# Kernel optimization log

Hardware: AMD Instinct MI355X
Metric: run time of the kernel (lower is better)

Reference implementation:

```python
import jax, jax.numpy as jnp
import numpy as np

EPS = 1e-5


def _prelu(x, a):
    return jnp.where(x >= 0, x, a * x)


def _chan_ln(x, gamma, beta, axis):
    # LayerNormalization4D: normalize over the channel axis, affine per channel
    mu = jnp.mean(x, axis=axis, keepdims=True)
    var = jnp.var(x, axis=axis, keepdims=True)
    return (x - mu) / jnp.sqrt(var + EPS) * gamma + beta


def setup_inputs() -> dict:
    key = jax.random.key(0)
    ks = jax.random.split(key, 12)
    B, C, T, F = 2, 64, 3000, 65
    H, D = 4, 4            # n_head, hid_chan
    E = C // H             # per-head value channels
    s = lambda k, shape: (jax.random.normal(k, shape, jnp.float32) * 0.05)
    return dict(
        x=jax.random.normal(ks[0], (B, C, T, F), jnp.float32),
        # per-head 1x1-conv Q/K/V projections (stacked over head axis)
        Wq=s(ks[1], (H, D, C)), bq=s(ks[2], (H, D)),
        aq=jnp.full((H,), 0.25, jnp.float32),
        gq=jnp.ones((H, D), jnp.float32), betaq=jnp.zeros((H, D), jnp.float32),
        Wk=s(ks[3], (H, D, C)), bk=s(ks[4], (H, D)),
        ak=jnp.full((H,), 0.25, jnp.float32),
        gk=jnp.ones((H, D), jnp.float32), betak=jnp.zeros((H, D), jnp.float32),
        Wv=s(ks[5], (H, E, C)), bv=s(ks[6], (H, E)),
        av=jnp.full((H,), 0.25, jnp.float32),
        gv=jnp.ones((H, E), jnp.float32), betav=jnp.zeros((H, E), jnp.float32),
        # final concat 1x1-conv projection
        Wp=s(ks[7], (C, C)), bp=s(ks[8], (C,)),
        ap=jnp.asarray(0.25, jnp.float32),
        gp=jnp.ones((C,), jnp.float32), betap=jnp.zeros((C,), jnp.float32),
    )


def _conv_act_norm_heads(x, W, b, a, g, beta):
    # x: [B,C,T,F]; W: [H,O,C] -> y: [B,H,O,T,F]
    y = jnp.einsum('hoc,bctf->bhotf', W, x) + b[None, :, :, None, None]
    y = _prelu(y, a[None, :, None, None, None])
    return _chan_ln(y, g[None, :, :, None, None], beta[None, :, :, None, None], axis=2)


def reference(x, Wq, bq, aq, gq, betaq, Wk, bk, ak, gk, betak,
              Wv, bv, av, gv, betav, Wp, bp, ap, gp, betap):
    B, C, T, F = x.shape
    H = Wq.shape[0]
    D = Wq.shape[1]
    E = Wv.shape[1]

    q = _conv_act_norm_heads(x, Wq, bq, aq, gq, betaq)   # [B,H,D,T,F]
    k = _conv_act_norm_heads(x, Wk, bk, ak, gk, betak)   # [B,H,D,T,F]
    v = _conv_act_norm_heads(x, Wv, bv, av, gv, betav)   # [B,H,E,T,F]

    # flatten (chan, freq) -> embedding per time step
    Qf = q.transpose(0, 1, 3, 2, 4).reshape(B, H, T, D * F)
    Kf = k.transpose(0, 1, 3, 2, 4).reshape(B, H, T, D * F)
    Vf = v.transpose(0, 1, 3, 2, 4).reshape(B, H, T, E * F)

    scale = 1.0 / jnp.sqrt(jnp.asarray(D * F, x.dtype))
    attn = jax.nn.softmax(jnp.einsum('bhtd,bhsd->bhts', Qf, Kf) * scale, axis=-1)
    o = jnp.einsum('bhts,bhse->bhte', attn, Vf)          # [B,H,T,E*F]

    # un-flatten and concat heads along channel dim
    o = o.reshape(B, H, T, E, F).transpose(0, 1, 3, 2, 4).reshape(B, H * E, T, F)

    # final 1x1 conv + PReLU + channel LN, then residual
    y = jnp.einsum('oc,bctf->botf', Wp, o) + bp[None, :, None, None]
    y = _prelu(y, ap)
    y = _chan_ln(y, gp[None, :, None, None], betap[None, :, None, None], axis=1)
    return y + x
```

## Files before the change

kernel.cpp:

```cpp
#include <hip/hip_runtime.h>
#include <stdint.h>

#define B_ 2
#define C_ 64
#define T_ 3000
#define F_ 65
#define H_ 4
#define D_ 4
#define E_ 16
#define TF_ (T_*F_)
#define NPT (B_*TF_)
#define EF 1040
#define TP 3072
#define TK 3008
#define DQK 260
#define SQK 328
#define VTROWS 1152
#define ABUF 8192
#define BBUF 4096

typedef unsigned short u16;
typedef unsigned int   u32;
typedef __attribute__((ext_vector_type(8))) short  s16x8;
typedef __attribute__((ext_vector_type(4))) float  f32x4;
typedef __attribute__((ext_vector_type(4))) u32    u32x4;

__device__ __forceinline__ float bf2f(u16 u){ return __uint_as_float(((u32)u)<<16); }
__device__ __forceinline__ float bf2f_lo(u32 u){ return __uint_as_float(u<<16); }
__device__ __forceinline__ float bf2f_hi(u32 u){ return __uint_as_float(u & 0xffff0000u); }
__device__ __forceinline__ u16 f2bf(float f){
  u32 u = __float_as_uint(f);
  u32 r = u + 0x7fffu + ((u>>16)&1u);
  return (u16)(r>>16);
}

__device__ __forceinline__ void gld16(const u16* g, u16* l){
  __builtin_amdgcn_global_load_lds((const __attribute__((address_space(1))) u32*)g,
                                   (__attribute__((address_space(3))) u32*)l,
                                   16, 0, 0);
}

__global__ __launch_bounds__(256) void qkv_kernel(
    const float* __restrict__ x,
    const float* __restrict__ Wq, const float* __restrict__ bq, const float* __restrict__ aq,
    const float* __restrict__ gq, const float* __restrict__ bteq,
    const float* __restrict__ Wk, const float* __restrict__ bk, const float* __restrict__ ak,
    const float* __restrict__ gk, const float* __restrict__ btek,
    const float* __restrict__ Wv, const float* __restrict__ bv, const float* __restrict__ av,
    const float* __restrict__ gv, const float* __restrict__ btev,
    u16* __restrict__ Qf, u16* __restrict__ Kf, u16* __restrict__ Vf,
    float* __restrict__ lbuf)
{
  __shared__ __align__(16) u16 wlds[2*96*64];
  const int tid = threadIdx.x;
  for (int i = tid; i < 6144; i += 256){
    const int row = i >> 6, c = i & 63;
    float w;
    if (row < 16)      w = Wq[row*64 + c];
    else if (row < 32) w = Wk[(row-16)*64 + c];
    else               w = Wv[(row-32)*64 + c];
    const u16 hi = f2bf(w);
    const u16 lo = f2bf(w - bf2f(hi));
    const int byo = ((row<<7) + (c<<1)) ^ ((row&7)<<4);
    *(u16*)((char*)wlds + byo)         = hi;
    *(u16*)((char*)wlds + 12288 + byo) = lo;
  }
  const int gid = blockIdx.x*256 + tid;
  if (gid < 8*TP) lbuf[gid] = 0.f;
  __syncthreads();

  const int wv_ = tid >> 6, l = tid & 63;
  const int lm = l & 15, lq = l >> 4;
  const int p0 = blockIdx.x*128 + wv_*32;

  int bb[2], rr[2]; bool ok[2];
  #pragma unroll
  for (int nt=0; nt<2; nt++){
    int p = p0 + nt*16 + lm;
    ok[nt] = (p < NPT);
    if (p >= NPT) p = NPT-1;
    bb[nt] = (p >= TF_) ? 1 : 0;
    rr[nt] = p - bb[nt]*TF_;
  }

  f32x4 acc[6][2];
  #pragma unroll
  for (int i=0;i<6;i++){
    acc[i][0]=(f32x4){0.f,0.f,0.f,0.f};
    acc[i][1]=(f32x4){0.f,0.f,0.f,0.f};
  }

  #pragma unroll
  for (int ks=0; ks<2; ks++){
    const int c0 = ks*32 + lq*8;
    s16x8 xhi[2], xlo[2];
    #pragma unroll
    for (int nt=0; nt<2; nt++){
      const float* xb = x + ((size_t)bb[nt]*C_ + c0)*TF_ + rr[nt];
      float xr[8];
      #pragma unroll
      for (int j=0;j<8;j++) xr[j] = xb[(size_t)j*TF_];
      u32x4 hw, lw;
      #pragma unroll
      for (int jw=0;jw<4;jw++){
        const u16 h0 = f2bf(xr[jw*2+0]);
        const u16 h1 = f2bf(xr[jw*2+1]);
        const float r0 = xr[jw*2+0] - bf2f(h0);
        const float r1 = xr[jw*2+1] - bf2f(h1);
        hw[jw] = (u32)h0 | ((u32)h1<<16);
        lw[jw] = (u32)f2bf(r0) | ((u32)f2bf(r1)<<16);
      }
      xhi[nt] = __builtin_bit_cast(s16x8, hw);
      xlo[nt] = __builtin_bit_cast(s16x8, lw);
    }
    #pragma unroll
    for (int mt=0; mt<6; mt++){
      const int rowb = mt*16 + lm;
      const int byo = ((rowb<<7) + (c0<<1)) ^ ((rowb&7)<<4);
      const s16x8 whi = *(const s16x8*)((const char*)wlds + byo);
      const s16x8 wlo = *(const s16x8*)((const char*)wlds + 12288 + byo);
      #pragma unroll
      for (int nt=0; nt<2; nt++){
        acc[mt][nt] = __builtin_amdgcn_mfma_f32_16x16x32_bf16(whi, xhi[nt], acc[mt][nt], 0,0,0);
        acc[mt][nt] = __builtin_amdgcn_mfma_f32_16x16x32_bf16(whi, xlo[nt], acc[mt][nt], 0,0,0);
        acc[mt][nt] = __builtin_amdgcn_mfma_f32_16x16x32_bf16(wlo, xhi[nt], acc[mt][nt], 0,0,0);
      }
    }
  }

  #pragma unroll
  for (int nt=0; nt<2; nt++){
    if (!ok[nt]) continue;
    const int b = bb[nt], r = rr[nt];
    const u32 t = (u32)(((unsigned long long)r * 516223ULL) >> 25);
    const int f = r - (int)t*65;
    {
      const int h = lq;
      const float a_ = aq[h];
      float v[4]; float s1 = 0.f;
      #pragma unroll
      for (int d=0; d<4; d++){
        float a = acc[0][nt][d] + bq[h*4+d];
        a = (a >= 0.f) ? a : a_*a;
        v[d] = a; s1 += a;
      }
      const float mu = s1*0.25f;
      float var = 0.f;
      #pragma unroll
      for (int d=0; d<4; d++){ const float dd = v[d]-mu; var = fmaf(dd,dd,var); }
      var *= 0.25f;
      const float rs = rsqrtf(var + 1e-5f);
      u16* qrow = Qf + ((size_t)(b*4+h)*TP + t)*SQK + f;
      #pragma unroll
      for (int d=0; d<4; d++)
        qrow[d*F_] = f2bf((v[d]-mu)*rs*gq[h*4+d] + bteq[h*4+d]);
    }
    {
      const int h = lq;
      const float a_ = ak[h];
      float v[4]; float s1 = 0.f;
      #pragma unroll
      for (int d=0; d<4; d++){
        float a = acc[1][nt][d] + bk[h*4+d];
        a = (a >= 0.f) ? a : a_*a;
        v[d] = a; s1 += a;
      }
      const float mu = s1*0.25f;
      float var = 0.f;
      #pragma unroll
      for (int d=0; d<4; d++){ const float dd = v[d]-mu; var = fmaf(dd,dd,var); }
      var *= 0.25f;
      const float rs = rsqrtf(var + 1e-5f);
      u16* krow = Kf + ((size_t)(b*4+h)*TP + t)*SQK + f;
      #pragma unroll
      for (int d=0; d<4; d++)
        krow[d*F_] = f2bf((v[d]-mu)*rs*gk[h*4+d] + btek[h*4+d]);
    }
    if (f < 28) {
      #pragma unroll
      for (int h2=0; h2<4; h2++){
        Qf[((size_t)(b*4+h2)*TP + t)*SQK + 260 + f] = 0;
        Kf[((size_t)(b*4+h2)*TP + t)*SQK + 260 + f] = 0;
      }
    }
    #pragma unroll
    for (int mt=2; mt<6; mt++){
      const int h = mt-2;
      const float a_ = av[h];
      float v[4]; float s1 = 0.f, s2 = 0.f;
      #pragma unroll
      for (int e4=0; e4<4; e4++){
        float a = acc[mt][nt][e4] + bv[h*16 + lq*4 + e4];
        a = (a >= 0.f) ? a : a_*a;
        v[e4] = a; s1 += a; s2 = fmaf(a,a,s2);
      }
      s1 += __shfl_xor(s1,16); s1 += __shfl_xor(s1,32);
      s2 += __shfl_xor(s2,16); s2 += __shfl_xor(s2,32);
      const float mu = s1*(1.f/16.f);
      const float var = s2*(1.f/16.f) - mu*mu;
      const float rs = rsqrtf(var + 1e-5f);
      u16* vrow = Vf + ((size_t)(b*4+h)*T_ + t)*EF + f;
      #pragma unroll
      for (int e4=0; e4<4; e4++){
        const int e = lq*4 + e4;
        vrow[e*F_] = f2bf((v[e4]-mu)*rs*gv[h*16+e] + btev[h*16+e]);
      }
    }
  }
}

__global__ __launch_bounds__(256) void vtrans_kernel(
    const u16* __restrict__ Vf, u16* __restrict__ Vt)
{
  __shared__ u16 tile[64][68];
  const int bh = blockIdx.z, t0 = blockIdx.x*64, c0 = blockIdx.y*64;
  const int tid = threadIdx.x;
  const int rr = tid>>4, cc4 = (tid&15)*4;
  #pragma unroll
  for (int i=0;i<4;i++){
    const int key = t0 + rr + i*16;
    ushort4 v = {0,0,0,0};
    if (key < T_) {
      const u16* src = Vf + ((size_t)bh*T_ + key)*EF + c0 + cc4;
      if (c0 + cc4 + 3 < EF) v = *(const ushort4*)src;
      else {
        if (c0+cc4+0 < EF) v.x = src[0];
        if (c0+cc4+1 < EF) v.y = src[1];
        if (c0+cc4+2 < EF) v.z = src[2];
        if (c0+cc4+3 < EF) v.w = src[3];
      }
    }
    *(ushort4*)&tile[rr + i*16][cc4] = v;
  }
  __syncthreads();
  #pragma unroll
  for (int i=0;i<4;i++){
    const int cl = rr + i*16;
    const int col = c0 + cl;
    ushort4 v;
    v.x = tile[cc4+0][cl];
    v.y = tile[cc4+1][cl];
    v.z = tile[cc4+2][cl];
    v.w = tile[cc4+3][cl];
    *(ushort4*)(Vt + ((size_t)bh*VTROWS + col)*TK + t0 + cc4) = v;
  }
}

__device__ __forceinline__ void gemm_core(
    const u16* __restrict__ Ag, const u16* __restrict__ Bg,
    size_t strideA, size_t strideB, int niter,
    u16* As, u16* Bs, f32x4 acc[4][4], int w, int l, int tid)
{
  const int sa1 = tid + 512;
  const int ra0 = tid>>2, ja0 = (tid&3) ^ ((ra0>>1)&3);
  const int ra1 = sa1>>2, ja1 = (sa1&3) ^ ((ra1>>1)&3);
  const int jb0 = (tid&3) ^ ((ra0>>1)&3);
  const u16* gA0 = Ag + (size_t)ra0*strideA + ja0*8;
  const u16* gA1 = Ag + (size_t)ra1*strideA + ja1*8;
  const u16* gB0 = Bg + (size_t)ra0*strideB + jb0*8;
  u16* lA0 = As + (size_t)(w*64)*8;
  u16* lA1 = As + (size_t)(512 + w*64)*8;
  u16* lB0 = Bs + (size_t)(w*64)*8;
  const int m = l & 15, q = l >> 4;
  const int sw = (q ^ ((m>>1)&3)) << 3;
  const int ra = (w&3)*64 + m;
  const int rb = (w>>2)*64 + m;

  #pragma unroll
  for (int t=0; t<3; ++t){
    if (t < niter){
      const int k0 = t*32;
      gld16(gA0 + k0, lA0 + t*ABUF);
      gld16(gA1 + k0, lA1 + t*ABUF);
      gld16(gB0 + k0, lB0 + t*BBUF);
    }
  }
  int cur = 0;
  for (int it = 0; it < niter; ++it) {
    if (it < niter-2)      asm volatile("s_waitcnt vmcnt(6)" ::: "memory");
    else if (it < niter-1) asm volatile("s_waitcnt vmcnt(3)" ::: "memory");
    else                   asm volatile("s_waitcnt vmcnt(0)" ::: "memory");
    __builtin_amdgcn_s_barrier();
    __builtin_amdgcn_sched_barrier(0);
    s16x8 a[4], b[4];
    #pragma unroll
    for (int i=0;i<4;i++) a[i] = *(const s16x8*)(As + cur*ABUF + (ra + i*16)*32 + sw);
    #pragma unroll
    for (int j=0;j<4;j++) b[j] = *(const s16x8*)(Bs + cur*BBUF + (rb + j*16)*32 + sw);
    #pragma unroll
    for (int i=0;i<4;i++)
      #pragma unroll
      for (int j=0;j<4;j++)
        acc[i][j] = __builtin_amdgcn_mfma_f32_16x16x32_bf16(a[i], b[j], acc[i][j], 0, 0, 0);
    __builtin_amdgcn_sched_barrier(0);
    __builtin_amdgcn_s_barrier();
    if (it + 3 < niter) {
      const int k0 = (it+3)*32;
      gld16(gA0 + k0, lA0 + cur*ABUF);
      gld16(gA1 + k0, lA1 + cur*ABUF);
      gld16(gB0 + k0, lB0 + cur*BBUF);
    }
    cur = (cur == 2) ? 0 : cur + 1;
  }
}

__global__ __launch_bounds__(512) void scores_kernel(
    const u16* __restrict__ Qf, const u16* __restrict__ Kf,
    u16* __restrict__ P, float* __restrict__ lbuf, int bh0)
{
  __shared__ __align__(16) u16 As[3*ABUF];
  __shared__ __align__(16) u16 Bs[3*BBUF];
  const int tid = threadIdx.x, w = tid>>6, l = tid&63;
  const int bh = bh0 + blockIdx.z;
  const int row0 = blockIdx.x*256, col0 = blockIdx.y*128;
  const u16* Ag = Qf + ((size_t)bh*TP + row0)*SQK;
  const u16* Bg = Kf + ((size_t)bh*TP + col0)*SQK;

  f32x4 acc[4][4];
  #pragma unroll
  for (int i=0;i<4;i++)
    #pragma unroll
    for (int j=0;j<4;j++) acc[i][j] = (f32x4){0.f,0.f,0.f,0.f};

  gemm_core(Ag, Bg, SQK, SQK, 9, As, Bs, acc, w, l, tid);

  const float scale = 0.062017367294604234f;
  const int m = l & 15, q = l >> 4;
  u16* Pz = P + (size_t)blockIdx.z*TP*TP;
  float* lrow = lbuf + (size_t)bh*TP;

  #pragma unroll
  for (int i=0;i<4;i++){
    #pragma unroll
    for (int reg=0; reg<4; reg++){
      const int grow = row0 + (w&3)*64 + i*16 + q*4 + reg;
      float rsum = 0.f;
      #pragma unroll
      for (int j=0;j<4;j++){
        const int gcol = col0 + (w>>2)*64 + j*16 + m;
        float pv = __expf(acc[i][j][reg]*scale);
        if (gcol >= T_) pv = 0.f;
        rsum += pv;
        Pz[(size_t)grow*TP + gcol] = f2bf(pv);
      }
      rsum += __shfl_xor(rsum, 8);
      rsum += __shfl_xor(rsum, 4);
      rsum += __shfl_xor(rsum, 2);
      rsum += __shfl_xor(rsum, 1);
      if (m == 0) atomicAdd(&lrow[grow], rsum);
    }
  }
}

__global__ __launch_bounds__(512) void pv_kernel(
    const u16* __restrict__ P, const u16* __restrict__ Vt,
    const float* __restrict__ lbuf, u16* __restrict__ Opt, int bh0)
{
  __shared__ __align__(16) u16 As[3*ABUF];
  __shared__ __align__(16) u16 Bs[3*BBUF];
  const int tid = threadIdx.x, w = tid>>6, l = tid&63;
  const int bh = bh0 + blockIdx.z;
  const int row0 = blockIdx.x*256, col0 = blockIdx.y*128;
  const u16* Ag = P + (size_t)blockIdx.z*TP*TP + (size_t)row0*TP;
  const u16* Bg = Vt + ((size_t)bh*VTROWS + col0)*TK;

  f32x4 acc[4][4];
  #pragma unroll
  for (int i=0;i<4;i++)
    #pragma unroll
    for (int j=0;j<4;j++) acc[i][j] = (f32x4){0.f,0.f,0.f,0.f};

  gemm_core(Ag, Bg, TP, TK, 94, As, Bs, acc, w, l, tid);

  const int m = l & 15, q = l >> 4;
  const float* lrow = lbuf + (size_t)bh*TP;
  const int b = bh >> 2, h = bh & 3;
  u16* Ob = Opt + (size_t)b*TF_*64 + h*16;

  #pragma unroll
  for (int i=0;i<4;i++){
    #pragma unroll
    for (int reg=0; reg<4; reg++){
      const int grow = row0 + (w&3)*64 + i*16 + q*4 + reg;
      if (grow >= T_) continue;
      const float linv = 1.0f / lrow[grow];
      #pragma unroll
      for (int j=0;j<4;j++){
        const int gcol = col0 + (w>>2)*64 + j*16 + m;
        if (gcol < EF) {
          const int e = (gcol*1009) >> 16;
          const int f = gcol - e*65;
          Ob[((size_t)grow*65 + f)*64 + e] = f2bf(acc[i][j][reg]*linv);
        }
      }
    }
  }
}

__global__ __launch_bounds__(256) void outp_kernel(
    const u16* __restrict__ Opt, const float* __restrict__ x,
    const float* __restrict__ Wp, const float* __restrict__ bp, const float* __restrict__ ap,
    const float* __restrict__ gp, const float* __restrict__ btep,
    float* __restrict__ out)
{
  __shared__ __align__(16) float4 wp4[1024];
  __shared__ float prm[193];
  const int tid = threadIdx.x;
  {
    const float4* wp = (const float4*)Wp;
    for (int i = tid; i < 1024; i += 256) wp4[i] = wp[i];
    if (tid < 193) {
      float v;
      if      (tid < 64)  v = bp[tid];
      else if (tid < 128) v = gp[tid-64];
      else if (tid < 192) v = btep[tid-128];
      else                v = ap[0];
      prm[tid] = v;
    }
  }
  __syncthreads();
  const int p0 = (blockIdx.x*256 + tid)*2;
  if (p0 >= NPT) return;
  const int b = p0 / TF_;
  const int r0 = p0 - b*TF_;

  float4 ov[2][16];
  #pragma unroll
  for (int np=0;np<2;np++){
    const uint4* op = (const uint4*)(Opt + (size_t)(p0+np)*64);
    #pragma unroll
    for (int i=0;i<8;i++){
      uint4 v = op[i];
      ov[np][i*2+0] = (float4){bf2f_lo(v.x), bf2f_hi(v.x), bf2f_lo(v.y), bf2f_hi(v.y)};
      ov[np][i*2+1] = (float4){bf2f_lo(v.z), bf2f_hi(v.z), bf2f_lo(v.w), bf2f_hi(v.w)};
    }
  }
  const float apv = prm[192];
  float ssum[2] = {0.f,0.f}, ssq[2] = {0.f,0.f};
  u32 ypk[2][32];
  #pragma unroll
  for (int o2=0; o2<32; o2++){
    float a0[2], a1[2];
    #pragma unroll
    for (int np=0;np<2;np++){ a0[np] = prm[o2*2]; a1[np] = prm[o2*2+1]; }
    #pragma unroll
    for (int c4=0; c4<16; c4++){
      float4 w0 = wp4[(o2*2)*16+c4];
      float4 w1 = wp4[(o2*2+1)*16+c4];
      #pragma unroll
      for (int np=0;np<2;np++){
        float4 xv = ov[np][c4];
        a0[np] = fmaf(w0.w,xv.w,fmaf(w0.z,xv.z,fmaf(w0.y,xv.y,fmaf(w0.x,xv.x,a0[np]))));
        a1[np] = fmaf(w1.w,xv.w,fmaf(w1.z,xv.z,fmaf(w1.y,xv.y,fmaf(w1.x,xv.x,a1[np]))));
      }
    }
    #pragma unroll
    for (int np=0;np<2;np++){
      float b0 = (a0[np] >= 0.f) ? a0[np] : apv*a0[np];
      float b1 = (a1[np] >= 0.f) ? a1[np] : apv*a1[np];
      ssum[np] += b0 + b1;
      ssq[np] = fmaf(b0,b0,fmaf(b1,b1,ssq[np]));
      ypk[np][o2] = (u32)f2bf(b0) | ((u32)f2bf(b1) << 16);
    }
  }
  float mu[2], rs[2];
  #pragma unroll
  for (int np=0;np<2;np++){
    mu[np] = ssum[np] * (1.f/64.f);
    float var = ssq[np] * (1.f/64.f) - mu[np]*mu[np];
    rs[np] = rsqrtf(var + 1e-5f);
  }
  const float* xb = x + (size_t)b*C_*TF_ + r0;
  float* yb = out + (size_t)b*C_*TF_ + r0;
  #pragma unroll
  for (int o2=0; o2<32; o2++){
    const int o = o2*2;
    const float y00 = bf2f_lo(ypk[0][o2]), y01 = bf2f_hi(ypk[0][o2]);
    const float y10 = bf2f_lo(ypk[1][o2]), y11 = bf2f_hi(ypk[1][o2]);
    const float2 xv0 = *(const float2*)(xb + (size_t)o*TF_);
    const float2 xv1 = *(const float2*)(xb + (size_t)(o+1)*TF_);
    float2 w0, w1;
    w0.x = fmaf((y00-mu[0])*rs[0], prm[64+o],   prm[128+o])   + xv0.x;
    w0.y = fmaf((y10-mu[1])*rs[1], prm[64+o],   prm[128+o])   + xv0.y;
    w1.x = fmaf((y01-mu[0])*rs[0], prm[64+o+1], prm[128+o+1]) + xv1.x;
    w1.y = fmaf((y11-mu[1])*rs[1], prm[64+o+1], prm[128+o+1]) + xv1.y;
    *(float2*)(yb + (size_t)o*TF_)     = w0;
    *(float2*)(yb + (size_t)(o+1)*TF_) = w1;
  }
}

extern "C" void kernel_launch(void* const* d_in, const int* in_sizes, int n_in,
                              void* d_out, int out_size, void* d_ws, size_t ws_size,
                              hipStream_t stream)
{
  const float* x    = (const float*)d_in[0];
  const float* Wq   = (const float*)d_in[1];
  const float* bq   = (const float*)d_in[2];
  const float* aq   = (const float*)d_in[3];
  const float* gq   = (const float*)d_in[4];
  const float* bteq = (const float*)d_in[5];
  const float* Wk   = (const float*)d_in[6];
  const float* bk   = (const float*)d_in[7];
  const float* ak   = (const float*)d_in[8];
  const float* gk   = (const float*)d_in[9];
  const float* btek = (const float*)d_in[10];
  const float* Wv   = (const float*)d_in[11];
  const float* bv   = (const float*)d_in[12];
  const float* av   = (const float*)d_in[13];
  const float* gv   = (const float*)d_in[14];
  const float* btev = (const float*)d_in[15];
  const float* Wp   = (const float*)d_in[16];
  const float* bp   = (const float*)d_in[17];
  const float* ap   = (const float*)d_in[18];
  const float* gp   = (const float*)d_in[19];
  const float* btep = (const float*)d_in[20];

  char* ws = (char*)d_ws;
  u16*   Qf   = (u16*)(ws + 0);
  u16*   Kf   = (u16*)(ws + 16121856);
  u16*   Vf   = (u16*)(ws + 32243712);
  u16*   Opt  = (u16*)(ws + 32243712);
  u16*   Vt   = (u16*)(ws + 82163712);
  const bool z4 = (ws_size >= (size_t)213202944);
  u16*   P;
  float* lbuf;
  if (z4) { lbuf = (float*)(ws + 137607168); P = (u16*)(ws + 137705472); }
  else    { P = (u16*)(ws + 137607168);      lbuf = (float*)(ws + 175355904); }
  float* out  = (float*)d_out;

  qkv_kernel<<<dim3((NPT+127)/128), dim3(256), 0, stream>>>(
      x, Wq,bq,aq,gq,bteq, Wk,bk,ak,gk,btek, Wv,bv,av,gv,btev, Qf,Kf,Vf, lbuf);
  vtrans_kernel<<<dim3(47, 17, 8), dim3(256), 0, stream>>>(Vf, Vt);
  if (z4) {
    for (int c = 0; c < 2; ++c) {
      scores_kernel<<<dim3(12, 24, 4), dim3(512), 0, stream>>>(Qf, Kf, P, lbuf, c*4);
      pv_kernel<<<dim3(12, 9, 4), dim3(512), 0, stream>>>(P, Vt, lbuf, Opt, c*4);
    }
  } else {
    for (int c = 0; c < 4; ++c) {
      scores_kernel<<<dim3(12, 24, 2), dim3(512), 0, stream>>>(Qf, Kf, P, lbuf, c*2);
      pv_kernel<<<dim3(12, 9, 2), dim3(512), 0, stream>>>(P, Vt, lbuf, Opt, c*2);
    }
  }
  outp_kernel<<<dim3((NPT/2+255)/256), dim3(256), 0, stream>>>(
      Opt, x, Wp,bp,ap,gp,btep, out);
}
```

Measured before the change: 828.7 us.

## Transpose scores tile for packed P stores and move output projection onto MFMA

The scores kernel swaps the roles of Q and K in the GEMM. Each lane then holds four consecutive columns of P and writes them as one 8-byte store, and each lane keeps a per-row partial sum that is reduced across lanes. The PV kernel now writes its output in the natural [b,h,t,e*f] layout with contiguous row stores, replacing the old scattered transpose stores. The output projection kernel computes the 64x64 channel mix with bf16 MFMA, splitting Wp into hi and lo bf16 parts to keep accuracy, and gathers its inputs with strided loads. The risk is uncoalesced gathers in outp and per-element stores to the output.

```diff
diff --git a/kernel.cpp b/kernel.cpp
--- a/kernel.cpp
+++ b/kernel.cpp
@@ -312,9 +312,9 @@
   __shared__ __align__(16) u16 Bs[3*BBUF];
   const int tid = threadIdx.x, w = tid>>6, l = tid&63;
   const int bh = bh0 + blockIdx.z;
-  const int row0 = blockIdx.x*256, col0 = blockIdx.y*128;
-  const u16* Ag = Qf + ((size_t)bh*TP + row0)*SQK;
-  const u16* Bg = Kf + ((size_t)bh*TP + col0)*SQK;
+  const int gcol0 = blockIdx.x*256, row0 = blockIdx.y*128;
+  const u16* Ag = Kf + ((size_t)bh*TP + gcol0)*SQK;
+  const u16* Bg = Qf + ((size_t)bh*TP + row0)*SQK;
 
   f32x4 acc[4][4];
   #pragma unroll
@@ -329,32 +329,37 @@
   u16* Pz = P + (size_t)blockIdx.z*TP*TP;
   float* lrow = lbuf + (size_t)bh*TP;
 
+  float rsum[4] = {0.f,0.f,0.f,0.f};
   #pragma unroll
   for (int i=0;i<4;i++){
-    #pragma unroll
-    for (int reg=0; reg<4; reg++){
-      const int grow = row0 + (w&3)*64 + i*16 + q*4 + reg;
-      float rsum = 0.f;
-      #pragma unroll
-      for (int j=0;j<4;j++){
-        const int gcol = col0 + (w>>2)*64 + j*16 + m;
-        float pv = __expf(acc[i][j][reg]*scale);
-        if (gcol >= T_) pv = 0.f;
-        rsum += pv;
-        Pz[(size_t)grow*TP + gcol] = f2bf(pv);
-      }
-      rsum += __shfl_xor(rsum, 8);
-      rsum += __shfl_xor(rsum, 4);
-      rsum += __shfl_xor(rsum, 2);
-      rsum += __shfl_xor(rsum, 1);
-      if (m == 0) atomicAdd(&lrow[grow], rsum);
-    }
+    const int gcb = gcol0 + (w&3)*64 + i*16 + q*4;
+    #pragma unroll
+    for (int j=0;j<4;j++){
+      const int grow = row0 + (w>>2)*64 + j*16 + m;
+      float pv[4];
+      #pragma unroll
+      for (int reg=0; reg<4; reg++){
+        float v = __expf(acc[i][j][reg]*scale);
+        if (gcb + reg >= T_) v = 0.f;
+        pv[reg] = v; rsum[j] += v;
+      }
+      const u32 lo = (u32)f2bf(pv[0]) | ((u32)f2bf(pv[1])<<16);
+      const u32 hi = (u32)f2bf(pv[2]) | ((u32)f2bf(pv[3])<<16);
+      *(uint2*)(Pz + (size_t)grow*TP + gcb) = make_uint2(lo, hi);
+    }
+  }
+  #pragma unroll
+  for (int j=0;j<4;j++){
+    float r = rsum[j];
+    r += __shfl_xor(r, 16);
+    r += __shfl_xor(r, 32);
+    if (q == 0) atomicAdd(&lrow[row0 + (w>>2)*64 + j*16 + m], r);
   }
 }
 
 __global__ __launch_bounds__(512) void pv_kernel(
     const u16* __restrict__ P, const u16* __restrict__ Vt,
-    const float* __restrict__ lbuf, u16* __restrict__ Opt, int bh0)
+    const float* __restrict__ lbuf, u16* __restrict__ Og, int bh0)
 {
   __shared__ __align__(16) u16 As[3*ABUF];
   __shared__ __align__(16) u16 Bs[3*BBUF];
@@ -374,8 +379,6 @@
 
   const int m = l & 15, q = l >> 4;
   const float* lrow = lbuf + (size_t)bh*TP;
-  const int b = bh >> 2, h = bh & 3;
-  u16* Ob = Opt + (size_t)b*TF_*64 + h*16;
 
   #pragma unroll
   for (int i=0;i<4;i++){
@@ -384,108 +387,131 @@
       const int grow = row0 + (w&3)*64 + i*16 + q*4 + reg;
       if (grow >= T_) continue;
       const float linv = 1.0f / lrow[grow];
+      u16* orow = Og + ((size_t)bh*T_ + grow)*EF;
       #pragma unroll
       for (int j=0;j<4;j++){
         const int gcol = col0 + (w>>2)*64 + j*16 + m;
-        if (gcol < EF) {
-          const int e = (gcol*1009) >> 16;
-          const int f = gcol - e*65;
-          Ob[((size_t)grow*65 + f)*64 + e] = f2bf(acc[i][j][reg]*linv);
-        }
+        if (gcol < EF)
+          orow[gcol] = f2bf(acc[i][j][reg]*linv);
       }
     }
   }
 }
 
 __global__ __launch_bounds__(256) void outp_kernel(
-    const u16* __restrict__ Opt, const float* __restrict__ x,
+    const u16* __restrict__ Og, const float* __restrict__ x,
     const float* __restrict__ Wp, const float* __restrict__ bp, const float* __restrict__ ap,
     const float* __restrict__ gp, const float* __restrict__ btep,
     float* __restrict__ out)
 {
-  __shared__ __align__(16) float4 wp4[1024];
+  __shared__ __align__(16) u16 wlds[2*64*64];
   __shared__ float prm[193];
   const int tid = threadIdx.x;
-  {
-    const float4* wp = (const float4*)Wp;
-    for (int i = tid; i < 1024; i += 256) wp4[i] = wp[i];
-    if (tid < 193) {
-      float v;
-      if      (tid < 64)  v = bp[tid];
-      else if (tid < 128) v = gp[tid-64];
-      else if (tid < 192) v = btep[tid-128];
-      else                v = ap[0];
-      prm[tid] = v;
-    }
+  for (int i = tid; i < 4096; i += 256){
+    const int row = i >> 6, c = i & 63;
+    const float w = Wp[row*64 + c];
+    const u16 hi = f2bf(w);
+    const u16 lo = f2bf(w - bf2f(hi));
+    const int byo = ((row<<7) + (c<<1)) ^ ((row&7)<<4);
+    *(u16*)((char*)wlds + byo)        = hi;
+    *(u16*)((char*)wlds + 8192 + byo) = lo;
+  }
+  if (tid < 193) {
+    float v;
+    if      (tid < 64)  v = bp[tid];
+    else if (tid < 128) v = gp[tid-64];
+    else if (tid < 192) v = btep[tid-128];
+    else                v = ap[0];
+    prm[tid] = v;
   }
   __syncthreads();
-  const int p0 = (blockIdx.x*256 + tid)*2;
-  if (p0 >= NPT) return;
-  const int b = p0 / TF_;
-  const int r0 = p0 - b*TF_;
-
-  float4 ov[2][16];
-  #pragma unroll
-  for (int np=0;np<2;np++){
-    const uint4* op = (const uint4*)(Opt + (size_t)(p0+np)*64);
-    #pragma unroll
-    for (int i=0;i<8;i++){
-      uint4 v = op[i];
-      ov[np][i*2+0] = (float4){bf2f_lo(v.x), bf2f_hi(v.x), bf2f_lo(v.y), bf2f_hi(v.y)};
-      ov[np][i*2+1] = (float4){bf2f_lo(v.z), bf2f_hi(v.z), bf2f_lo(v.w), bf2f_hi(v.w)};
-    }
-  }
+
+  const int wv_ = tid >> 6, l = tid & 63;
+  const int lm = l & 15, lq = l >> 4;
+  const int p0 = blockIdx.x*128 + wv_*32;
+
+  int bb[2], rr[2], tt[2], ff[2]; bool ok[2];
+  #pragma unroll
+  for (int nt=0; nt<2; nt++){
+    int p = p0 + nt*16 + lm;
+    ok[nt] = (p < NPT);
+    if (p >= NPT) p = NPT-1;
+    bb[nt] = (p >= TF_) ? 1 : 0;
+    rr[nt] = p - bb[nt]*TF_;
+    tt[nt] = (int)(((unsigned long long)rr[nt] * 516223ULL) >> 25);
+    ff[nt] = rr[nt] - tt[nt]*65;
+  }
+
+  f32x4 acc[4][2];
+  #pragma unroll
+  for (int i=0;i<4;i++){
+    acc[i][0]=(f32x4){0.f,0.f,0.f,0.f};
+    acc[i][1]=(f32x4){0.f,0.f,0.f,0.f};
+  }
+
+  #pragma unroll
+  for (int ks=0; ks<2; ks++){
+    const int c0 = ks*32 + lq*8;
+    const int h  = c0 >> 4;
+    const int e0 = c0 & 15;
+    s16x8 xf[2];
+    #pragma unroll
+    for (int nt=0; nt<2; nt++){
+      const u16* base = Og + ((size_t)(bb[nt]*4 + h)*T_ + tt[nt])*EF + ff[nt];
+      u32x4 pk;
+      #pragma unroll
+      for (int jw=0; jw<4; jw++){
+        const u16 v0 = base[(e0 + jw*2 + 0)*65];
+        const u16 v1 = base[(e0 + jw*2 + 1)*65];
+        pk[jw] = (u32)v0 | ((u32)v1 << 16);
+      }
+      xf[nt] = __builtin_bit_cast(s16x8, pk);
+    }
+    #pragma unroll
+    for (int mt=0; mt<4; mt++){
+      const int rowb = mt*16 + lm;
+      const int byo = ((rowb<<7) + (c0<<1)) ^ ((rowb&7)<<4);
+      const s16x8 whi = *(const s16x8*)((const char*)wlds + byo);
+      const s16x8 wlo = *(const s16x8*)((const char*)wlds + 8192 + byo);
+      #pragma unroll
+      for (int nt=0; nt<2; nt++){
+        acc[mt][nt] = __builtin_amdgcn_mfma_f32_16x16x32_bf16(whi, xf[nt], acc[mt][nt], 0,0,0);
+        acc[mt][nt] = __builtin_amdgcn_mfma_f32_16x16x32_bf16(wlo, xf[nt], acc[mt][nt], 0,0,0);
+      }
+    }
+  }
+
   const float apv = prm[192];
-  float ssum[2] = {0.f,0.f}, ssq[2] = {0.f,0.f};
-  u32 ypk[2][32];
-  #pragma unroll
-  for (int o2=0; o2<32; o2++){
-    float a0[2], a1[2];
-    #pragma unroll
-    for (int np=0;np<2;np++){ a0[np] = prm[o2*2]; a1[np] = prm[o2*2+1]; }
-    #pragma unroll
-    for (int c4=0; c4<16; c4++){
-      float4 w0 = wp4[(o2*2)*16+c4];
-      float4 w1 = wp4[(o2*2+1)*16+c4];
-      #pragma unroll
-      for (int np=0;np<2;np++){
-        float4 xv = ov[np][c4];
-        a0[np] = fmaf(w0.w,xv.w,fmaf(w0.z,xv.z,fmaf(w0.y,xv.y,fmaf(w0.x,xv.x,a0[np]))));
-        a1[np] = fmaf(w1.w,xv.w,fmaf(w1.z,xv.z,fmaf(w1.y,xv.y,fmaf(w1.x,xv.x,a1[np]))));
-      }
-    }
-    #pragma unroll
-    for (int np=0;np<2;np++){
-      float b0 = (a0[np] >= 0.f) ? a0[np] : apv*a0[np];
-      float b1 = (a1[np] >= 0.f) ? a1[np] : apv*a1[np];
-      ssum[np] += b0 + b1;
-      ssq[np] = fmaf(b0,b0,fmaf(b1,b1,ssq[np]));
-      ypk[np][o2] = (u32)f2bf(b0) | ((u32)f2bf(b1) << 16);
-    }
-  }
-  float mu[2], rs[2];
-  #pragma unroll
-  for (int np=0;np<2;np++){
-    mu[np] = ssum[np] * (1.f/64.f);
-    float var = ssq[np] * (1.f/64.f) - mu[np]*mu[np];
-    rs[np] = rsqrtf(var + 1e-5f);
-  }
-  const float* xb = x + (size_t)b*C_*TF_ + r0;
-  float* yb = out + (size_t)b*C_*TF_ + r0;
-  #pragma unroll
-  for (int o2=0; o2<32; o2++){
-    const int o = o2*2;
-    const float y00 = bf2f_lo(ypk[0][o2]), y01 = bf2f_hi(ypk[0][o2]);
-    const float y10 = bf2f_lo(ypk[1][o2]), y11 = bf2f_hi(ypk[1][o2]);
-    const float2 xv0 = *(const float2*)(xb + (size_t)o*TF_);
-    const float2 xv1 = *(const float2*)(xb + (size_t)(o+1)*TF_);
-    float2 w0, w1;
-    w0.x = fmaf((y00-mu[0])*rs[0], prm[64+o],   prm[128+o])   + xv0.x;
-    w0.y = fmaf((y10-mu[1])*rs[1], prm[64+o],   prm[128+o])   + xv0.y;
-    w1.x = fmaf((y01-mu[0])*rs[0], prm[64+o+1], prm[128+o+1]) + xv1.x;
-    w1.y = fmaf((y11-mu[1])*rs[1], prm[64+o+1], prm[128+o+1]) + xv1.y;
-    *(float2*)(yb + (size_t)o*TF_)     = w0;
-    *(float2*)(yb + (size_t)(o+1)*TF_) = w1;
+  #pragma unroll
+  for (int nt=0; nt<2; nt++){
+    if (!ok[nt]) continue;
+    const int b = bb[nt], r = rr[nt];
+    float v[4][4]; float s1 = 0.f, s2 = 0.f;
+    #pragma unroll
+    for (int mt=0; mt<4; mt++){
+      #pragma unroll
+      for (int reg=0; reg<4; reg++){
+        const int o = mt*16 + lq*4 + reg;
+        float a = acc[mt][nt][reg] + prm[o];
+        a = (a >= 0.f) ? a : apv*a;
+        v[mt][reg] = a; s1 += a; s2 = fmaf(a,a,s2);
+      }
+    }
+    s1 += __shfl_xor(s1,16); s1 += __shfl_xor(s1,32);
+    s2 += __shfl_xor(s2,16); s2 += __shfl_xor(s2,32);
+    const float mu = s1*(1.f/64.f);
+    const float var = s2*(1.f/64.f) - mu*mu;
+    const float rs = rsqrtf(var + 1e-5f);
+    const float* xb = x + (size_t)b*C_*TF_ + r;
+    float* yb = out + (size_t)b*C_*TF_ + r;
+    #pragma unroll
+    for (int mt=0; mt<4; mt++){
+      #pragma unroll
+      for (int reg=0; reg<4; reg++){
+        const int o = mt*16 + lq*4 + reg;
+        yb[(size_t)o*TF_] = fmaf((v[mt][reg]-mu)*rs, prm[64+o], prm[128+o]) + xb[(size_t)o*TF_];
+      }
+    }
   }
 }
 
@@ -519,7 +545,7 @@
   u16*   Qf   = (u16*)(ws + 0);
   u16*   Kf   = (u16*)(ws + 16121856);
   u16*   Vf   = (u16*)(ws + 32243712);
-  u16*   Opt  = (u16*)(ws + 32243712);
+  u16*   Og   = (u16*)(ws + 32243712);
   u16*   Vt   = (u16*)(ws + 82163712);
   const bool z4 = (ws_size >= (size_t)213202944);
   u16*   P;
@@ -534,14 +560,14 @@
   if (z4) {
     for (int c = 0; c < 2; ++c) {
       scores_kernel<<<dim3(12, 24, 4), dim3(512), 0, stream>>>(Qf, Kf, P, lbuf, c*4);
-      pv_kernel<<<dim3(12, 9, 4), dim3(512), 0, stream>>>(P, Vt, lbuf, Opt, c*4);
+      pv_kernel<<<dim3(12, 9, 4), dim3(512), 0, stream>>>(P, Vt, lbuf, Og, c*4);
     }
   } else {
     for (int c = 0; c < 4; ++c) {
       scores_kernel<<<dim3(12, 24, 2), dim3(512), 0, stream>>>(Qf, Kf, P, lbuf, c*2);
-      pv_kernel<<<dim3(12, 9, 2), dim3(512), 0, stream>>>(P, Vt, lbuf, Opt, c*2);
-    }
-  }
-  outp_kernel<<<dim3((NPT/2+255)/256), dim3(256), 0, stream>>>(
-      Opt, x, Wp,bp,ap,gp,btep, out);
-}
+      pv_kernel<<<dim3(12, 9, 2), dim3(512), 0, stream>>>(P, Vt, lbuf, Og, c*2);
+    }
+  }
+  outp_kernel<<<dim3((NPT+127)/128), dim3(256), 0, stream>>>(
+      Og, x, Wp,bp,ap,gp,btep, out);
+}
```

Measured after the change: 684.6 us. -17.4%, faster.
